# Performance work log

Measured on AMD Instinct MI355X. Metric: run time of the kernel, lower is better.

Reference implementation:

```python
import jax, jax.numpy as jnp
import numpy as np

NUM_VOXELS = 1_000_000
N_POINTS = 1_500_000
TOTAL_PROP_PTS = 1_000_000
NUM_PROPOSALS = 2048
IN_CH = 134  # 3 + 3 + 128
M = 16       # backbone output width
BATCH = 8


def setup_inputs() -> dict:
    key = jax.random.key(0)
    k1, k2, k3, k4, k5, k6 = jax.random.split(key, 6)
    voxel_feats = jax.random.normal(k1, (NUM_VOXELS, IN_CH), dtype=jnp.float32)
    W = jax.random.normal(k2, (IN_CH, M), dtype=jnp.float32) * 0.05
    p2v_map = jax.random.randint(k3, (N_POINTS,), 0, NUM_VOXELS, dtype=jnp.int64)
    # column 0: proposal id (unused), column 1: point index into pt_feats
    col1 = jax.random.randint(k4, (TOTAL_PROP_PTS,), 0, N_POINTS, dtype=jnp.int64)
    gt_proposals_idx = jnp.stack([jnp.zeros_like(col1), col1], axis=1)
    interior = jnp.sort(jax.random.randint(k5, (NUM_PROPOSALS - 1,), 0, TOTAL_PROP_PTS, dtype=jnp.int64))
    gt_proposals_offset = jnp.concatenate([
        jnp.zeros((1,), jnp.int64), interior,
        jnp.full((1,), TOTAL_PROP_PTS, jnp.int64)])
    # column 0 is the batch (scene) id
    locs_scaled = jax.random.randint(k6, (N_POINTS, 4), 0, BATCH, dtype=jnp.int32)
    return {
        'voxel_feats': voxel_feats,
        'W': W,
        'p2v_map': p2v_map,
        'gt_proposals_idx': gt_proposals_idx,
        'gt_proposals_offset': gt_proposals_offset,
        'locs_scaled': locs_scaled,
    }


def reference(voxel_feats, W, p2v_map, gt_proposals_idx, gt_proposals_offset, locs_scaled):
    # Stand-in for the Minkowski sparse backbone: pointwise projection + ReLU, 134 -> 16.
    feats = jax.nn.relu(voxel_feats @ W)                 # (V, 16)
    pt_feats = feats[p2v_map]                            # (N, 16) voxel->point gather

    P = gt_proposals_offset.shape[0] - 1
    point_idx = gt_proposals_idx[:, 1]                   # (T,)
    T = point_idx.shape[0]

    # CSR offsets -> segment ids (replaces the Python loop over proposals)
    seg_ids = jnp.searchsorted(gt_proposals_offset, jnp.arange(T), side='right') - 1

    gathered = pt_feats[point_idx]                       # (T, 16) ragged gather
    sums = jax.ops.segment_sum(gathered, seg_ids, num_segments=P)
    counts = jax.ops.segment_sum(jnp.ones((T,), feats.dtype), seg_ids, num_segments=P)
    proposal_feats = sums / jnp.maximum(counts, 1.0)[:, None]   # (P, 16) segment mean

    batch_idxs = locs_scaled[:, 0]                       # (N,) scene ids
    proposals_batchId = batch_idxs[point_idx][gt_proposals_offset[:-1]]  # (P,)
    proposal_objectness_scores = jnp.ones((P,), dtype=bool)
    return proposal_feats, proposals_batchId, proposal_objectness_scores
```

## Files before the change

### kernel.cpp

```cpp
#include <hip/hip_runtime.h>

#define NUM_VOXELS     1000000
#define N_POINTS       1500000
#define TOTAL_PROP_PTS 1000000
#define NUM_PROPOSALS  2048
#define IN_CH          134
#define M_OUT          16

__global__ __launch_bounds__(256, 2) void k_gemm_relu(
    const float* __restrict__ A, const float* __restrict__ W,
    float* __restrict__ feats)
{
    __shared__ float lds[4][64 * 65];
    const int wave = threadIdx.x >> 6;
    const int lane = threadIdx.x & 63;
    const int v0   = blockIdx.x * 256 + wave * 64;
    if (v0 >= NUM_VOXELS) return;

    float* chunk = lds[wave];
    float acc[M_OUT];
#pragma unroll
    for (int c = 0; c < M_OUT; ++c) acc[c] = 0.f;

    for (int kc = 0; kc < IN_CH; kc += 64) {
        const int KC = (IN_CH - kc) >= 64 ? 64 : (IN_CH - kc);
        if (KC == 64) {
            const int half = lane >> 5;
            const int c2   = (lane & 31) * 2;
#pragma unroll 4
            for (int j = 0; j < 32; ++j) {
                const int row = j * 2 + half;
                const float2 val = *(const float2*)(A + (size_t)(v0 + row) * IN_CH + kc + c2);
                chunk[row * 65 + c2]     = val.x;
                chunk[row * 65 + c2 + 1] = val.y;
            }
        } else {
#pragma unroll
            for (int j = 0; j < 6; ++j) {
                const int e   = j * 64 + lane;
                const int row = e / 6;
                const int col = e - row * 6;
                chunk[row * 65 + col] = A[(size_t)(v0 + row) * IN_CH + kc + col];
            }
        }
        const float* wbase = W + kc * M_OUT;
        for (int kk = 0; kk < KC; ++kk) {
            const float a = chunk[lane * 65 + kk];
            const float* wr = wbase + kk * M_OUT;
#pragma unroll
            for (int c = 0; c < M_OUT; ++c) acc[c] = fmaf(a, wr[c], acc[c]);
        }
    }

    float4* orow = (float4*)(feats + (size_t)(v0 + lane) * M_OUT);
#pragma unroll
    for (int q = 0; q < 4; ++q) {
        float4 o;
        o.x = fmaxf(acc[q * 4 + 0], 0.f);
        o.y = fmaxf(acc[q * 4 + 1], 0.f);
        o.z = fmaxf(acc[q * 4 + 2], 0.f);
        o.w = fmaxf(acc[q * 4 + 3], 0.f);
        orow[q] = o;
    }
}

__global__ __launch_bounds__(256) void k_propmean(
    const float* __restrict__ feats,
    const int*   __restrict__ p2v,
    const int*   __restrict__ prop_idx,
    const int*   __restrict__ offsets,
    const int*   __restrict__ locs,
    float*       __restrict__ out)
{
    const int s   = blockIdx.x;
    const int tid = threadIdx.x;
    const int t0  = offsets[s];
    const int t1  = offsets[s + 1];

    float acc[M_OUT];
#pragma unroll
    for (int c = 0; c < M_OUT; ++c) acc[c] = 0.f;

    for (int t = t0 + tid; t < t1; t += 256) {
        const int p = prop_idx[2 * t + 1];
        const int v = p2v[p];
        const float4* fp = (const float4*)(feats + (size_t)v * M_OUT);
        const float4 f0 = fp[0], f1 = fp[1], f2 = fp[2], f3 = fp[3];
        acc[0]  += f0.x; acc[1]  += f0.y; acc[2]  += f0.z; acc[3]  += f0.w;
        acc[4]  += f1.x; acc[5]  += f1.y; acc[6]  += f1.z; acc[7]  += f1.w;
        acc[8]  += f2.x; acc[9]  += f2.y; acc[10] += f2.z; acc[11] += f2.w;
        acc[12] += f3.x; acc[13] += f3.y; acc[14] += f3.z; acc[15] += f3.w;
    }

#pragma unroll
    for (int c = 0; c < M_OUT; ++c) {
#pragma unroll
        for (int off = 32; off > 0; off >>= 1)
            acc[c] += __shfl_down(acc[c], off, 64);
    }

    __shared__ float red[4][M_OUT];
    const int lane = tid & 63, wv = tid >> 6;
    if (lane == 0) {
#pragma unroll
        for (int c = 0; c < M_OUT; ++c) red[wv][c] = acc[c];
    }
    __syncthreads();

    if (tid < M_OUT) {
        const float sum = red[0][tid] + red[1][tid] + red[2][tid] + red[3][tid];
        const float cnt = (float)(t1 - t0);
        out[s * M_OUT + tid] = sum / fmaxf(cnt, 1.f);
    }
    if (tid == 0) {
        const int p = prop_idx[2 * t0 + 1];
        out[NUM_PROPOSALS * M_OUT + s]                 = (float)locs[4 * p];
        out[NUM_PROPOSALS * M_OUT + NUM_PROPOSALS + s] = 1.0f;
    }
}

extern "C" void kernel_launch(void* const* d_in, const int* in_sizes, int n_in,
                              void* d_out, int out_size, void* d_ws, size_t ws_size,
                              hipStream_t stream)
{
    const float* A    = (const float*)d_in[0];
    const float* W    = (const float*)d_in[1];
    const int*   p2v  = (const int*)  d_in[2];
    const int*   pidx = (const int*)  d_in[3];
    const int*   offs = (const int*)  d_in[4];
    const int*   locs = (const int*)  d_in[5];
    float*       out  = (float*)      d_out;
    float*       feats = (float*)     d_ws;

    k_gemm_relu<<<(NUM_VOXELS + 255) / 256, 256, 0, stream>>>(A, W, feats);
    k_propmean<<<NUM_PROPOSALS, 256, 0, stream>>>(feats, p2v, pidx, offs, locs, out);
}
```

Before: 791.9 us.

## Register double-buffer GEMM input tiles and prefetch gather indices in proposal mean

The GEMM kernel now stages A in 32-column chunks through registers. The next chunk is loaded while the current one is consumed from LDS. The 6 tail columns are loaded directly per lane and handled separately. The LDS footprint is halved and the occupancy hint is raised to 4 blocks. The proposal-mean kernel software-pipelines the index→voxel lookup one iteration ahead and reads the index pair as int2, to hide dependent-load latency. In exchange, register pressure rises (16 float2 buffers) and the chunk loads are only 8-byte per lane, with row strides that may coalesce poorly.

```diff
diff --git a/kernel.cpp b/kernel.cpp
--- a/kernel.cpp
+++ b/kernel.cpp
@@ -7,48 +7,73 @@
 #define IN_CH          134
 #define M_OUT          16
 
-__global__ __launch_bounds__(256, 2) void k_gemm_relu(
+__global__ __launch_bounds__(256, 4) void k_gemm_relu(
     const float* __restrict__ A, const float* __restrict__ W,
     float* __restrict__ feats)
 {
-    __shared__ float lds[4][64 * 65];
+    __shared__ float lds[4][64 * 33];
     const int wave = threadIdx.x >> 6;
     const int lane = threadIdx.x & 63;
     const int v0   = blockIdx.x * 256 + wave * 64;
     if (v0 >= NUM_VOXELS) return;
 
     float* chunk = lds[wave];
+
+    const float* myrow = A + (size_t)(v0 + lane) * IN_CH;
+    const float2 tl0 = *(const float2*)(myrow + 128);
+    const float2 tl1 = *(const float2*)(myrow + 130);
+    const float2 tl2 = *(const float2*)(myrow + 132);
+
+    const int srow = lane >> 4;
+    const int scol = (lane & 15) * 2;
+    const float* sbase = A + (size_t)(v0 + srow) * IN_CH + scol;
+
+    float2 buf[16];
+#pragma unroll
+    for (int j = 0; j < 16; ++j)
+        buf[j] = *(const float2*)(sbase + (size_t)j * 4 * IN_CH);
+
     float acc[M_OUT];
 #pragma unroll
     for (int c = 0; c < M_OUT; ++c) acc[c] = 0.f;
 
-    for (int kc = 0; kc < IN_CH; kc += 64) {
-        const int KC = (IN_CH - kc) >= 64 ? 64 : (IN_CH - kc);
-        if (KC == 64) {
-            const int half = lane >> 5;
-            const int c2   = (lane & 31) * 2;
-#pragma unroll 4
-            for (int j = 0; j < 32; ++j) {
-                const int row = j * 2 + half;
-                const float2 val = *(const float2*)(A + (size_t)(v0 + row) * IN_CH + kc + c2);
-                chunk[row * 65 + c2]     = val.x;
-                chunk[row * 65 + c2 + 1] = val.y;
-            }
-        } else {
 #pragma unroll
-            for (int j = 0; j < 6; ++j) {
-                const int e   = j * 64 + lane;
-                const int row = e / 6;
-                const int col = e - row * 6;
-                chunk[row * 65 + col] = A[(size_t)(v0 + row) * IN_CH + kc + col];
-            }
+    for (int cidx = 0; cidx < 4; ++cidx) {
+        const int kc = cidx * 32;
+
+#pragma unroll
+        for (int j = 0; j < 16; ++j) {
+            const int row = j * 4 + srow;
+            *(float2*)&chunk[row * 33 + scol] = buf[j];
         }
+
+        if (cidx < 3) {
+            const float* nb = sbase + kc + 32;
+#pragma unroll
+            for (int j = 0; j < 16; ++j)
+                buf[j] = *(const float2*)(nb + (size_t)j * 4 * IN_CH);
+        }
+
         const float* wbase = W + kc * M_OUT;
-        for (int kk = 0; kk < KC; ++kk) {
-            const float a = chunk[lane * 65 + kk];
+#pragma unroll
+        for (int kk = 0; kk < 32; ++kk) {
+            const float a = chunk[lane * 33 + kk];
             const float* wr = wbase + kk * M_OUT;
 #pragma unroll
             for (int c = 0; c < M_OUT; ++c) acc[c] = fmaf(a, wr[c], acc[c]);
+        }
+    }
+
+    {
+        const float* wr = W + 128 * M_OUT;
+#pragma unroll
+        for (int c = 0; c < M_OUT; ++c) {
+            float v = fmaf(tl0.x, wr[0 * M_OUT + c], acc[c]);
+            v = fmaf(tl0.y, wr[1 * M_OUT + c], v);
+            v = fmaf(tl1.x, wr[2 * M_OUT + c], v);
+            v = fmaf(tl1.y, wr[3 * M_OUT + c], v);
+            v = fmaf(tl2.x, wr[4 * M_OUT + c], v);
+            acc[c] = fmaf(tl2.y, wr[5 * M_OUT + c], v);
         }
     }
 
@@ -76,20 +101,31 @@
     const int tid = threadIdx.x;
     const int t0  = offsets[s];
     const int t1  = offsets[s + 1];
+    const int2* pidx2 = (const int2*)prop_idx;
 
     float acc[M_OUT];
 #pragma unroll
     for (int c = 0; c < M_OUT; ++c) acc[c] = 0.f;
 
-    for (int t = t0 + tid; t < t1; t += 256) {
-        const int p = prop_idx[2 * t + 1];
-        const int v = p2v[p];
+    int t = t0 + tid;
+    bool have = (t < t1);
+    int v = 0;
+    if (have) v = p2v[pidx2[t].y];
+
+    while (have) {
+        const int  tn     = t + 256;
+        const bool have_n = (tn < t1);
+        int vn = 0;
+        if (have_n) vn = p2v[pidx2[tn].y];
+
         const float4* fp = (const float4*)(feats + (size_t)v * M_OUT);
         const float4 f0 = fp[0], f1 = fp[1], f2 = fp[2], f3 = fp[3];
         acc[0]  += f0.x; acc[1]  += f0.y; acc[2]  += f0.z; acc[3]  += f0.w;
         acc[4]  += f1.x; acc[5]  += f1.y; acc[6]  += f1.z; acc[7]  += f1.w;
         acc[8]  += f2.x; acc[9]  += f2.y; acc[10] += f2.z; acc[11] += f2.w;
         acc[12] += f3.x; acc[13] += f3.y; acc[14] += f3.z; acc[15] += f3.w;
+
+        v = vn; t = tn; have = have_n;
     }
 
 #pragma unroll
```

Measured after the change: 774.3 us. 1.02x faster.
